# Optimization experiments

Measured on AMD Instinct MI355X. Metric: run time of the kernel, lower is better.

The kernel has to match this reference:

```python
import jax, jax.numpy as jnp
import numpy as np

B, T, D = 64, 512, 512
K_CODES = 256
K_FUTURE = 2


def _gru(x, w_ih, w_hh, b_ih, b_hh):
    # x: [B,T,D]; PyTorch GRU gate order: r, z, n; weights [3D, D]
    xg = jnp.einsum('btd,gd->btg', x, w_ih) + b_ih  # [B,T,3D] precomputed input gates

    def step(h, xg_t):
        hg = h @ w_hh.T + b_hh                      # [B,3D]
        xr, xz, xn = jnp.split(xg_t, 3, axis=-1)
        hr, hz, hn = jnp.split(hg, 3, axis=-1)
        r = jax.nn.sigmoid(xr + hr)
        z = jax.nn.sigmoid(xz + hz)
        n = jnp.tanh(xn + r * hn)
        h_new = (1.0 - z) * n + z * h
        return h_new, h_new

    h0 = jnp.zeros((x.shape[0], w_hh.shape[1]), x.dtype)
    _, hs = jax.lax.scan(step, h0, jnp.swapaxes(xg, 0, 1))
    return jnp.swapaxes(hs, 0, 1)  # [B,T,D]


def setup_inputs() -> dict:
    key = jax.random.key(0)
    ks = jax.random.split(key, 8)
    return {
        'features': jax.random.normal(ks[0], (B, T, D), jnp.float32),
        'codebook': jax.random.uniform(ks[1], (K_CODES, D), jnp.float32, -0.1, 0.1),
        'w_ih': jax.random.normal(ks[2], (3 * D, D), jnp.float32) * 0.02,
        'w_hh': jax.random.normal(ks[3], (3 * D, D), jnp.float32) * 0.02,
        'b_ih': jax.random.normal(ks[4], (3 * D,), jnp.float32) * 0.02,
        'b_hh': jax.random.normal(ks[5], (3 * D,), jnp.float32) * 0.02,
        'proj_w': jax.random.normal(ks[6], (D, D), jnp.float32) * 0.02,
        'proj_b': jax.random.normal(ks[7], (D,), jnp.float32) * 0.02,
    }


def reference(features, codebook, w_ih, w_hh, b_ih, b_hh, proj_w, proj_b):
    b, t, d = features.shape
    # --- quantize: cdist + argmin + gather (squared dists give same argmin) ---
    flat = features.reshape(-1, d)                              # [B*T, D]
    d2 = (jnp.sum(flat * flat, axis=1, keepdims=True)
          - 2.0 * flat @ codebook.T
          + jnp.sum(codebook * codebook, axis=1))               # [B*T, K]
    indices = jnp.argmin(d2, axis=1)                            # [B*T]
    quantized = codebook[indices].reshape(b, t, d)              # gather
    indices = indices.reshape(b, t)

    # --- context prediction loss ---
    hidden = _gru(quantized, w_ih, w_hh, b_ih, b_hh)            # [B,T,D]
    context_proj = hidden @ proj_w.T + proj_b                   # [B,T,D]
    k_max = min(K_FUTURE, t - 1)
    cp_loss = jnp.float32(0.0)
    for k in range(1, k_max + 1):
        cp_loss = cp_loss + jnp.mean((context_proj[:, :-k] - features[:, k:]) ** 2)
    cp_loss = cp_loss / k_max

    # --- VQ loss (stop_gradient mirrors torch .detach()) ---
    commitment_loss = jnp.mean((jax.lax.stop_gradient(features) - quantized) ** 2)
    codebook_loss = jnp.mean((features - jax.lax.stop_gradient(quantized)) ** 2)
    vq_loss = commitment_loss + 0.25 * codebook_loss

    total_loss = cp_loss + vq_loss
    return quantized, indices, total_loss, cp_loss, vq_loss
```

## Files before the change

kernel.cpp:

```cpp
#include <hip/hip_runtime.h>
#include <hip/hip_bf16.h>

#define B_ 64
#define T_ 512
#define D_ 512
#define K_ 256
#define G3 1536

typedef __attribute__((ext_vector_type(8))) short sh8;
typedef __attribute__((ext_vector_type(4))) short sh4;
typedef __attribute__((ext_vector_type(4))) float fx4;
typedef __attribute__((ext_vector_type(4))) int   ix4;

__device__ __forceinline__ short f2bf(float x) {
  __hip_bfloat16 h = __float2bfloat16(x);
  union { __hip_bfloat16 h; short s; } u; u.h = h; return u.s;
}
__device__ __forceinline__ float sigm(float x) { return 1.f / (1.f + __expf(-x)); }
__device__ __forceinline__ float tanh_fast(float x) {
  float e2 = __expf(-2.f * x);
  return (1.f - e2) / (1.f + e2);
}

__global__ void k_cnorm(const float* __restrict__ cb, double* __restrict__ cn) {
  int c = threadIdx.x;
  if (c < K_) {
    double s = 0.0;
    for (int k = 0; k < D_; ++k) { double v = cb[c * D_ + k]; s += v * v; }
    cn[c] = s;
  }
}

__global__ __launch_bounds__(256) void k_cg(const float* __restrict__ cb,
                                            const float* __restrict__ wih,
                                            const float* __restrict__ bih,
                                            const float* __restrict__ bhh,
                                            float* __restrict__ cg) {
  __shared__ float wl[16][512];
  int j0 = blockIdx.x * 16, c0 = blockIdx.y * 64;
  for (int v = threadIdx.x; v < 16 * 128; v += 256) {
    int r = v >> 7, q = v & 127;
    *(fx4*)&wl[r][q * 4] = *(const fx4*)&wih[(j0 + r) * D_ + q * 4];
  }
  __syncthreads();
  for (int p = threadIdx.x; p < 1024; p += 256) {
    int j = p >> 6, c = c0 + (p & 63);
    fx4 a = {0.f, 0.f, 0.f, 0.f};
    const float* cbr = &cb[c * D_];
    for (int q = 0; q < 128; ++q) {
      fx4 w4 = *(fx4*)&wl[j][q * 4];
      fx4 c4 = *(const fx4*)&cbr[q * 4];
      a += w4 * c4;
    }
    int jg = j0 + j;
    float bias = bih[jg] + (jg < 1024 ? bhh[jg] : 0.f);
    cg[c * G3 + jg] = ((a.x + a.y) + (a.z + a.w)) + bias;
  }
}

__global__ void k_cvt(const float* __restrict__ src, __hip_bfloat16* __restrict__ dst, int n4) {
  int i = blockIdx.x * blockDim.x + threadIdx.x;
  if (i < n4) {
    fx4 v = *(const fx4*)&src[i * 4];
    sh4 o; o[0] = f2bf(v.x); o[1] = f2bf(v.y); o[2] = f2bf(v.z); o[3] = f2bf(v.w);
    *(sh4*)&dst[i * 4] = o;
  }
}

__global__ __launch_bounds__(256) void k_quant(const float* __restrict__ feat,
                                               const float* __restrict__ cb,
                                               const double* __restrict__ cn,
                                               int* __restrict__ idxw,
                                               float* __restrict__ outq,
                                               float* __restrict__ outi,
                                               double* __restrict__ lacc) {
  __shared__ float fl[16][516];
  __shared__ double ss1[16][16], ss2[16][16];
  __shared__ int ii1[16][16], ii2[16][16];
  __shared__ int idxl[16];
  __shared__ float rsv[4];
  int row0 = blockIdx.x * 16;
  int tid = threadIdx.x;
  for (int v = tid; v < 16 * 128; v += 256) {
    int r = v >> 7, q = v & 127;
    *(fx4*)&fl[r][q * 4] = *(const fx4*)&feat[(row0 + r) * D_ + q * 4];
  }
  __syncthreads();
  int r = tid & 15, g = tid >> 4;
  fx4 acc[16];
#pragma unroll
  for (int c = 0; c < 16; ++c) acc[c] = (fx4){0.f, 0.f, 0.f, 0.f};
  for (int ch = 0; ch < 8; ++ch) {
    fx4 fc[16];
#pragma unroll
    for (int q = 0; q < 16; ++q) fc[q] = *(fx4*)&fl[r][ch * 64 + q * 4];
#pragma unroll
    for (int c = 0; c < 16; ++c) {
      const float* cbp = &cb[(g * 16 + c) * D_ + ch * 64];
#pragma unroll
      for (int q = 0; q < 16; ++q) {
        fx4 c4 = *(const fx4*)&cbp[q * 4];
        acc[c] += fc[q] * c4;
      }
    }
  }
  double b1 = 1e300, b2 = 1e300; int i1 = 0, i2 = 0;
#pragma unroll
  for (int c = 0; c < 16; ++c) {
    int ci = g * 16 + c;
    double dot = (double)acc[c].x + acc[c].y + acc[c].z + acc[c].w;
    double s = cn[ci] - 2.0 * dot;
    if (s < b1) { b2 = b1; i2 = i1; b1 = s; i1 = ci; }
    else if (s < b2) { b2 = s; i2 = ci; }
  }
  ss1[r][g] = b1; ss2[r][g] = b2; ii1[r][g] = i1; ii2[r][g] = i2;
  __syncthreads();
  if (tid < 16) {
    int rr = tid;
    double c1 = 1e300, c2 = 1e300; int j1 = 0, j2 = 0;
    for (int g2 = 0; g2 < 16; ++g2) {
      double s = ss1[rr][g2]; int ix = ii1[rr][g2];
      if (s < c1 || (s == c1 && ix < j1)) { c2 = c1; j2 = j1; c1 = s; j1 = ix; }
      else if (s < c2 || (s == c2 && ix < j2)) { c2 = s; j2 = ix; }
      s = ss2[rr][g2]; ix = ii2[rr][g2];
      if (s < c1 || (s == c1 && ix < j1)) { c2 = c1; j2 = j1; c1 = s; j1 = ix; }
      else if (s < c2 || (s == c2 && ix < j2)) { c2 = s; j2 = ix; }
    }
    int pick = j1;
    if (c2 - c1 < 1e-4) {
      double d1 = 0.0, d2 = 0.0;
      for (int k = 0; k < D_; ++k) {
        double fv = fl[rr][k];
        d1 += fv * (double)cb[j1 * D_ + k];
        d2 += fv * (double)cb[j2 * D_ + k];
      }
      double e1 = cn[j1] - 2.0 * d1, e2 = cn[j2] - 2.0 * d2;
      if (e2 < e1 || (e2 == e1 && j2 < j1)) pick = j2;
    }
    idxl[rr] = pick;
    idxw[row0 + rr] = pick;
    outi[row0 + rr] = (float)pick;
  }
  __syncthreads();
  float vs = 0.f;
  for (int v = tid; v < 16 * 128; v += 256) {
    int rr = v >> 7, q = v & 127;
    fx4 c4 = *(const fx4*)&cb[idxl[rr] * D_ + q * 4];
    *(fx4*)&outq[(row0 + rr) * D_ + q * 4] = c4;
    fx4 f4 = *(fx4*)&fl[rr][q * 4];
    fx4 d = f4 - c4;
    vs += d.x * d.x + d.y * d.y + d.z * d.z + d.w * d.w;
  }
#pragma unroll
  for (int off = 32; off > 0; off >>= 1) vs += __shfl_down(vs, off);
  if ((tid & 63) == 0) rsv[tid >> 6] = vs;
  __syncthreads();
  if (tid == 0) atomicAdd(&lacc[2], (double)(rsv[0] + rsv[1] + rsv[2] + rsv[3]));
}

__global__ __launch_bounds__(256, 1) void k_gru(const float* __restrict__ whh,
                                                const float* __restrict__ bhh,
                                                const float* __restrict__ cg,
                                                const int* __restrict__ idx,
                                                const __hip_bfloat16* __restrict__ pwb,
                                                const float* __restrict__ pb,
                                                const float* __restrict__ feat,
                                                __hip_bfloat16* __restrict__ hex,
                                                double* __restrict__ lacc,
                                                unsigned int* __restrict__ bar,
                                                unsigned int* __restrict__ coord) {
  int tid = threadIdx.x;
  __shared__ int sh_role, sh_fast;

  if (tid == 0) {
    int xcc = 0;
    asm volatile("s_getreg_b32 %0, hwreg(HW_REG_XCC_ID)" : "=s"(xcc));
    xcc &= 7;
    unsigned slot = __hip_atomic_fetch_add(&coord[xcc], 1u, __ATOMIC_RELAXED,
                                           __HIP_MEMORY_SCOPE_AGENT);
    __hip_atomic_fetch_add(&coord[16], 1u, __ATOMIC_ACQ_REL, __HIP_MEMORY_SCOPE_AGENT);
    while (__hip_atomic_load(&coord[16], __ATOMIC_ACQUIRE, __HIP_MEMORY_SCOPE_AGENT)
           < (unsigned)gridDim.x)
      __builtin_amdgcn_s_sleep(2);
    int role = -1;
    if (slot < 8u) {
      role = xcc * 8 + (int)slot;
    } else {
      for (int x = 0; x < 8 && role < 0; ++x) {
        unsigned cx = __hip_atomic_load(&coord[x], __ATOMIC_RELAXED,
                                        __HIP_MEMORY_SCOPE_AGENT);
        unsigned have = cx < 8u ? cx : 8u;
        if (have < 8u) {
          unsigned s2 = __hip_atomic_fetch_add(&coord[8 + x], 1u, __ATOMIC_RELAXED,
                                               __HIP_MEMORY_SCOPE_AGENT);
          if (s2 < 8u - have) role = x * 8 + (int)(have + s2);
        }
      }
    }
    sh_role = role;
    int fst = 0;
    if (role >= 0) {
      unsigned cgx = __hip_atomic_load(&coord[role >> 3], __ATOMIC_RELAXED,
                                       __HIP_MEMORY_SCOPE_AGENT);
      fst = (cgx >= 8u) ? 1 : 0;
    }
    sh_fast = fst;
    __threadfence();
  }
  __syncthreads();
  const int role = sh_role;
  if (role < 0) return;
  const bool fast = (sh_fast != 0);
  const int g = role >> 3, s = role & 7;

  int w = tid >> 6, lane = tid & 63, l15 = lane & 15, l4 = lane >> 4;

  sh8 A0[16], A1[16], A2[16];
#pragma unroll
  for (int kt = 0; kt < 16; ++kt) {
#pragma unroll
    for (int t3 = 0; t3 < 3; ++t3) {
      int lr = 48 * w + 16 * t3 + l15;
      int gate = lr >> 6, din = lr & 63;
      const float* wr = &whh[(gate * 512 + s * 64 + din) * D_];
      int k0 = kt * 32 + l4 * 8;
      fx4 x = *(const fx4*)&wr[k0];
      fx4 y = *(const fx4*)&wr[k0 + 4];
      sh8 tt;
      tt[0] = f2bf(x.x); tt[1] = f2bf(x.y); tt[2] = f2bf(x.z); tt[3] = f2bf(x.w);
      tt[4] = f2bf(y.x); tt[5] = f2bf(y.y); tt[6] = f2bf(y.z); tt[7] = f2bf(y.w);
      if (t3 == 0) A0[kt] = tt; else if (t3 == 1) A1[kt] = tt; else A2[kt] = tt;
    }
  }
  sh8 P[16];
#pragma unroll
  for (int kt = 0; kt < 16; ++kt)
    P[kt] = *(const sh8*)&pwb[(size_t)(s * 64 + w * 16 + l15) * D_ + kt * 32 + l4 * 8];

  const bool act = (l15 < 8);
  const int bp = l15 & 7;
  const int dgp = s * 64 + w * 16 + l4 * 4;
  fx4 pbv = *(const fx4*)&pb[dgp];

  const int d = tid & 63, b0 = tid >> 6, b1 = b0 + 4;
  const float bn = bhh[1024 + s * 64 + d];

  __shared__ float hg[192][9];
  __shared__ float hl[8][64];
  for (int i = tid; i < 512; i += 256) ((float*)hl)[i] = 0.f;

  unsigned* const barg = &bar[g * 32];
  float s1 = 0.f, s2 = 0.f;

  for (int t = 0; t < T_; ++t) {
    int cur = t & 1, nxt = cur ^ 1;
    int ci0 = idx[(g * 8 + b0) * T_ + t];
    int ci1 = idx[(g * 8 + b1) * T_ + t];
    const float* c0p = &cg[(size_t)ci0 * G3 + s * 64 + d];
    const float* c1p = &cg[(size_t)ci1 * G3 + s * 64 + d];
    float cr0 = c0p[0], cz0 = c0p[512], cn0 = c0p[1024];
    float cr1 = c1p[0], cz1 = c1p[512], cn1 = c1p[1024];

    fx4 a0 = {0, 0, 0, 0}, a1 = {0, 0, 0, 0}, a2 = {0, 0, 0, 0};
    fx4 pacc = {0, 0, 0, 0};
    if (t > 0) {
      const __hip_bfloat16* hb = hex + (size_t)(cur * 8 + g) * 16 * 512;
#pragma unroll
      for (int kt = 0; kt < 16; ++kt) {
        sh8 bfr = *(const sh8*)&hb[l15 * 512 + kt * 32 + l4 * 8];
        a0 = __builtin_amdgcn_mfma_f32_16x16x32_bf16(A0[kt], bfr, a0, 0, 0, 0);
        a1 = __builtin_amdgcn_mfma_f32_16x16x32_bf16(A1[kt], bfr, a1, 0, 0, 0);
        a2 = __builtin_amdgcn_mfma_f32_16x16x32_bf16(A2[kt], bfr, a2, 0, 0, 0);
        pacc = __builtin_amdgcn_mfma_f32_16x16x32_bf16(P[kt], bfr, pacc, 0, 0, 0);
      }
    }
    if (l15 < 8) {
#pragma unroll
      for (int rg = 0; rg < 4; ++rg) {
        hg[48 * w +      l4 * 4 + rg][l15] = a0[rg];
        hg[48 * w + 16 + l4 * 4 + rg][l15] = a1[rg];
        hg[48 * w + 32 + l4 * 4 + rg][l15] = a2[rg];
      }
    }
    __syncthreads();
    {
      float rr = sigm(cr0 + hg[d][b0]);
      float zz = sigm(cz0 + hg[64 + d][b0]);
      float nn = tanh_fast(cn0 + rr * (hg[128 + d][b0] + bn));
      float hv = (1.f - zz) * nn + zz * hl[b0][d];
      hl[b0][d] = hv;
      hex[(size_t)((nxt * 8 + g) * 16 + b0) * 512 + s * 64 + d] = __float2bfloat16(hv);
      rr = sigm(cr1 + hg[d][b1]);
      zz = sigm(cz1 + hg[64 + d][b1]);
      nn = tanh_fast(cn1 + rr * (hg[128 + d][b1] + bn));
      hv = (1.f - zz) * nn + zz * hl[b1][d];
      hl[b1][d] = hv;
      hex[(size_t)((nxt * 8 + g) * 16 + b1) * 512 + s * 64 + d] = __float2bfloat16(hv);
    }
    __syncthreads();
    if (tid == 0) {
      if (!fast) __threadfence();
      __hip_atomic_fetch_add(barg, 1u, __ATOMIC_RELEASE, __HIP_MEMORY_SCOPE_AGENT);
    }
    if (t > 0 && act) {
      fx4 f1 = *(const fx4*)&feat[((size_t)(g * 8 + bp) * T_ + t) * D_ + dgp];
      fx4 v = pacc + pbv;
      fx4 d1 = v - f1;
      s1 += d1.x * d1.x + d1.y * d1.y + d1.z * d1.z + d1.w * d1.w;
      if (t < T_ - 1) {
        fx4 f2 = *(const fx4*)&feat[((size_t)(g * 8 + bp) * T_ + t + 1) * D_ + dgp];
        fx4 d2 = v - f2;
        s2 += d2.x * d2.x + d2.y * d2.y + d2.z * d2.z + d2.w * d2.w;
      }
    }
    if (tid == 0) {
      unsigned tgt = 8u * (unsigned)(t + 1);
      while (__hip_atomic_load(barg, __ATOMIC_ACQUIRE, __HIP_MEMORY_SCOPE_AGENT) < tgt)
        __builtin_amdgcn_s_sleep(1);
      if (!fast) __threadfence();
    }
    __syncthreads();
  }

#pragma unroll
  for (int off = 32; off > 0; off >>= 1) {
    s1 += __shfl_down(s1, off);
    s2 += __shfl_down(s2, off);
  }
  __shared__ float r1[4], r2[4];
  if (lane == 0) { r1[w] = s1; r2[w] = s2; }
  __syncthreads();
  if (tid == 0) {
    atomicAdd(&lacc[0], (double)r1[0] + r1[1] + r1[2] + r1[3]);
    atomicAdd(&lacc[1], (double)r2[0] + r2[1] + r2[2] + r2[3]);
  }
}

__global__ void k_fin(const double* __restrict__ lacc, float* __restrict__ outl) {
  if (threadIdx.x == 0) {
    double cp = 0.5 * (lacc[0] / ((double)B_ * (T_ - 1) * D_) +
                       lacc[1] / ((double)B_ * (T_ - 2) * D_));
    double vq = 1.25 * lacc[2] / ((double)B_ * T_ * D_);
    outl[0] = (float)(cp + vq);
    outl[1] = (float)cp;
    outl[2] = (float)vq;
  }
}

extern "C" void kernel_launch(void* const* d_in, const int* in_sizes, int n_in,
                              void* d_out, int out_size, void* d_ws, size_t ws_size,
                              hipStream_t stream) {
  (void)in_sizes; (void)n_in; (void)out_size; (void)ws_size;
  const float* feat = (const float*)d_in[0];
  const float* cb   = (const float*)d_in[1];
  const float* wih  = (const float*)d_in[2];
  const float* whh  = (const float*)d_in[3];
  const float* bih  = (const float*)d_in[4];
  const float* bhh  = (const float*)d_in[5];
  const float* pw   = (const float*)d_in[6];
  const float* pb   = (const float*)d_in[7];

  float* out  = (float*)d_out;
  float* outq = out;
  float* outi = out + (size_t)B_ * T_ * D_;
  float* outl = outi + B_ * T_;

  char* ws = (char*)d_ws;
  size_t o = 0;
  auto alloc = [&](size_t sz) { void* p = ws + o; o += (sz + 255) & ~(size_t)255; return p; };
  float*          cg    = (float*)alloc(sizeof(float) * K_ * G3);
  double*         cn    = (double*)alloc(sizeof(double) * K_);
  int*            idxw  = (int*)alloc(sizeof(int) * B_ * T_);
  __hip_bfloat16* pwb   = (__hip_bfloat16*)alloc(sizeof(__hip_bfloat16) * D_ * D_);
  double*         lacc  = (double*)alloc(sizeof(double) * 4);
  unsigned*       bar   = (unsigned*)alloc(sizeof(unsigned) * 8 * 32);
  unsigned*       coord = (unsigned*)alloc(sizeof(unsigned) * 32);
  __hip_bfloat16* hex   = (__hip_bfloat16*)alloc(sizeof(__hip_bfloat16) * 2 * 8 * 16 * 512);

  hipMemsetAsync(lacc,  0, sizeof(double) * 4, stream);
  hipMemsetAsync(bar,   0, sizeof(unsigned) * 8 * 32, stream);
  hipMemsetAsync(coord, 0, sizeof(unsigned) * 32, stream);
  hipMemsetAsync(hex,   0, sizeof(__hip_bfloat16) * 2 * 8 * 16 * 512, stream);

  hipLaunchKernelGGL(k_cnorm, dim3(1), dim3(256), 0, stream, cb, cn);
  hipLaunchKernelGGL(k_cg, dim3(96, 4), dim3(256), 0, stream, cb, wih, bih, bhh, cg);
  hipLaunchKernelGGL(k_cvt, dim3(256), dim3(256), 0, stream, pw, pwb, D_ * D_ / 4);
  hipLaunchKernelGGL(k_quant, dim3(2048), dim3(256), 0, stream, feat, cb, cn, idxw, outq, outi, lacc);
  hipLaunchKernelGGL(k_gru, dim3(64), dim3(256), 0, stream, whh, bhh, cg, idxw, pwb, pb, feat, hex, lacc, bar, coord);
  hipLaunchKernelGGL(k_fin, dim3(1), dim3(64), 0, stream, lacc, outl);
}
```

Measured before the change: 3.440 ms.

## Replace per-step group barrier with per-slice flags and rotated K-order consumption

Each of the 8 GRU blocks in a group now publishes its own timestep flag instead of joining a counter barrier. Consumers start the recurrent matmul on their own slice from local shared memory, then poll each peer's flag in rotated order and consume that slice as soon as it is ready. The trailing barrier wait and the extra syncthreads are removed, and feature loads are hoisted ahead of the matmul. This aims to overlap peer latency with MFMA work and shrink the serial sync cost per timestep, at the price of more polling traffic and a subtler memory-ordering protocol. It also relies on the double-buffered hex slots never being overwritten early, since there is no longer a full barrier between steps.

```diff
diff --git a/kernel.cpp b/kernel.cpp
--- a/kernel.cpp
+++ b/kernel.cpp
@@ -167,7 +167,7 @@
                                                 const float* __restrict__ feat,
                                                 __hip_bfloat16* __restrict__ hex,
                                                 double* __restrict__ lacc,
-                                                unsigned int* __restrict__ bar,
+                                                unsigned int* __restrict__ flag,
                                                 unsigned int* __restrict__ coord) {
   int tid = threadIdx.x;
   __shared__ int sh_role, sh_fast;
@@ -215,27 +215,27 @@
 
   int w = tid >> 6, lane = tid & 63, l15 = lane & 15, l4 = lane >> 4;
 
-  sh8 A0[16], A1[16], A2[16];
-#pragma unroll
-  for (int kt = 0; kt < 16; ++kt) {
+  sh8 A0[16], A1[16], A2[16], P[16];
+#pragma unroll
+  for (int p = 0; p < 16; ++p) {
+    int jpos = p >> 1;
+    int j = (s + jpos) & 7;
+    int kt = 2 * j + (p & 1);
+    int k0 = kt * 32 + l4 * 8;
 #pragma unroll
     for (int t3 = 0; t3 < 3; ++t3) {
       int lr = 48 * w + 16 * t3 + l15;
       int gate = lr >> 6, din = lr & 63;
       const float* wr = &whh[(gate * 512 + s * 64 + din) * D_];
-      int k0 = kt * 32 + l4 * 8;
       fx4 x = *(const fx4*)&wr[k0];
       fx4 y = *(const fx4*)&wr[k0 + 4];
       sh8 tt;
       tt[0] = f2bf(x.x); tt[1] = f2bf(x.y); tt[2] = f2bf(x.z); tt[3] = f2bf(x.w);
       tt[4] = f2bf(y.x); tt[5] = f2bf(y.y); tt[6] = f2bf(y.z); tt[7] = f2bf(y.w);
-      if (t3 == 0) A0[kt] = tt; else if (t3 == 1) A1[kt] = tt; else A2[kt] = tt;
-    }
-  }
-  sh8 P[16];
-#pragma unroll
-  for (int kt = 0; kt < 16; ++kt)
-    P[kt] = *(const sh8*)&pwb[(size_t)(s * 64 + w * 16 + l15) * D_ + kt * 32 + l4 * 8];
+      if (t3 == 0) A0[p] = tt; else if (t3 == 1) A1[p] = tt; else A2[p] = tt;
+    }
+    P[p] = *(const sh8*)&pwb[(size_t)(s * 64 + w * 16 + l15) * D_ + k0];
+  }
 
   const bool act = (l15 < 8);
   const int bp = l15 & 7;
@@ -246,10 +246,9 @@
   const float bn = bhh[1024 + s * 64 + d];
 
   __shared__ float hg[192][9];
-  __shared__ float hl[8][64];
-  for (int i = tid; i < 512; i += 256) ((float*)hl)[i] = 0.f;
-
-  unsigned* const barg = &bar[g * 32];
+  __shared__ float hl[8][76];
+  for (int i = tid; i < 8 * 76; i += 256) ((float*)hl)[i] = 0.f;
+
   float s1 = 0.f, s2 = 0.f;
 
   for (int t = 0; t < T_; ++t) {
@@ -260,20 +259,60 @@
     const float* c1p = &cg[(size_t)ci1 * G3 + s * 64 + d];
     float cr0 = c0p[0], cz0 = c0p[512], cn0 = c0p[1024];
     float cr1 = c1p[0], cz1 = c1p[512], cn1 = c1p[1024];
+    fx4 f1 = {0, 0, 0, 0}, f2v = {0, 0, 0, 0};
+    if (t > 0 && act) {
+      f1 = *(const fx4*)&feat[((size_t)(g * 8 + bp) * T_ + t) * D_ + dgp];
+      if (t < T_ - 1)
+        f2v = *(const fx4*)&feat[((size_t)(g * 8 + bp) * T_ + t + 1) * D_ + dgp];
+    }
 
     fx4 a0 = {0, 0, 0, 0}, a1 = {0, 0, 0, 0}, a2 = {0, 0, 0, 0};
     fx4 pacc = {0, 0, 0, 0};
     if (t > 0) {
-      const __hip_bfloat16* hb = hex + (size_t)(cur * 8 + g) * 16 * 512;
-#pragma unroll
-      for (int kt = 0; kt < 16; ++kt) {
-        sh8 bfr = *(const sh8*)&hb[l15 * 512 + kt * 32 + l4 * 8];
-        a0 = __builtin_amdgcn_mfma_f32_16x16x32_bf16(A0[kt], bfr, a0, 0, 0, 0);
-        a1 = __builtin_amdgcn_mfma_f32_16x16x32_bf16(A1[kt], bfr, a1, 0, 0, 0);
-        a2 = __builtin_amdgcn_mfma_f32_16x16x32_bf16(A2[kt], bfr, a2, 0, 0, 0);
-        pacc = __builtin_amdgcn_mfma_f32_16x16x32_bf16(P[kt], bfr, pacc, 0, 0, 0);
-      }
-    }
+      unsigned vch = __hip_atomic_load(&flag[(g * 8 + (lane & 7)) * 32],
+                                       __ATOMIC_ACQUIRE, __HIP_MEMORY_SCOPE_AGENT);
+      unsigned mask = (unsigned)__ballot((int)(vch >= (unsigned)t)) & 0xffu;
+      if (!fast) __threadfence();
+
+#pragma unroll
+      for (int sub = 0; sub < 2; ++sub) {
+        sh8 bfr = {0, 0, 0, 0, 0, 0, 0, 0};
+        if (act) {
+          const float* hp = &hl[bp][sub * 32 + l4 * 8];
+#pragma unroll
+          for (int q = 0; q < 8; ++q) bfr[q] = f2bf(hp[q]);
+        }
+        a0 = __builtin_amdgcn_mfma_f32_16x16x32_bf16(A0[sub], bfr, a0, 0, 0, 0);
+        a1 = __builtin_amdgcn_mfma_f32_16x16x32_bf16(A1[sub], bfr, a1, 0, 0, 0);
+        a2 = __builtin_amdgcn_mfma_f32_16x16x32_bf16(A2[sub], bfr, a2, 0, 0, 0);
+        pacc = __builtin_amdgcn_mfma_f32_16x16x32_bf16(P[sub], bfr, pacc, 0, 0, 0);
+      }
+
+      const __hip_bfloat16* hb = hex + ((size_t)(cur * 8 + g) * 8 + bp) * 512;
+#pragma unroll
+      for (int jj = 1; jj < 8; ++jj) {
+        int j = (s + jj) & 7;
+        if (!((mask >> j) & 1u)) {
+          while (__hip_atomic_load(&flag[(g * 8 + j) * 32], __ATOMIC_ACQUIRE,
+                                   __HIP_MEMORY_SCOPE_AGENT) < (unsigned)t)
+            __builtin_amdgcn_s_sleep(1);
+          if (!fast) __threadfence();
+        }
+        asm volatile("" ::: "memory");
+#pragma unroll
+        for (int sub = 0; sub < 2; ++sub) {
+          int p = 2 * jj + sub;
+          int kt = 2 * j + sub;
+          sh8 bfr = {0, 0, 0, 0, 0, 0, 0, 0};
+          if (act) bfr = *(const sh8*)&hb[kt * 32 + l4 * 8];
+          a0 = __builtin_amdgcn_mfma_f32_16x16x32_bf16(A0[p], bfr, a0, 0, 0, 0);
+          a1 = __builtin_amdgcn_mfma_f32_16x16x32_bf16(A1[p], bfr, a1, 0, 0, 0);
+          a2 = __builtin_amdgcn_mfma_f32_16x16x32_bf16(A2[p], bfr, a2, 0, 0, 0);
+          pacc = __builtin_amdgcn_mfma_f32_16x16x32_bf16(P[p], bfr, pacc, 0, 0, 0);
+        }
+      }
+    }
+
     if (l15 < 8) {
 #pragma unroll
       for (int rg = 0; rg < 4; ++rg) {
@@ -289,37 +328,27 @@
       float nn = tanh_fast(cn0 + rr * (hg[128 + d][b0] + bn));
       float hv = (1.f - zz) * nn + zz * hl[b0][d];
       hl[b0][d] = hv;
-      hex[(size_t)((nxt * 8 + g) * 16 + b0) * 512 + s * 64 + d] = __float2bfloat16(hv);
+      hex[((size_t)(nxt * 8 + g) * 8 + b0) * 512 + s * 64 + d] = __float2bfloat16(hv);
       rr = sigm(cr1 + hg[d][b1]);
       zz = sigm(cz1 + hg[64 + d][b1]);
       nn = tanh_fast(cn1 + rr * (hg[128 + d][b1] + bn));
       hv = (1.f - zz) * nn + zz * hl[b1][d];
       hl[b1][d] = hv;
-      hex[(size_t)((nxt * 8 + g) * 16 + b1) * 512 + s * 64 + d] = __float2bfloat16(hv);
+      hex[((size_t)(nxt * 8 + g) * 8 + b1) * 512 + s * 64 + d] = __float2bfloat16(hv);
     }
     __syncthreads();
-    if (tid == 0) {
-      if (!fast) __threadfence();
-      __hip_atomic_fetch_add(barg, 1u, __ATOMIC_RELEASE, __HIP_MEMORY_SCOPE_AGENT);
-    }
+    if (tid == 0)
+      __hip_atomic_store(&flag[(g * 8 + s) * 32], (unsigned)(t + 1),
+                         __ATOMIC_RELEASE, __HIP_MEMORY_SCOPE_AGENT);
     if (t > 0 && act) {
-      fx4 f1 = *(const fx4*)&feat[((size_t)(g * 8 + bp) * T_ + t) * D_ + dgp];
       fx4 v = pacc + pbv;
       fx4 d1 = v - f1;
       s1 += d1.x * d1.x + d1.y * d1.y + d1.z * d1.z + d1.w * d1.w;
       if (t < T_ - 1) {
-        fx4 f2 = *(const fx4*)&feat[((size_t)(g * 8 + bp) * T_ + t + 1) * D_ + dgp];
-        fx4 d2 = v - f2;
+        fx4 d2 = v - f2v;
         s2 += d2.x * d2.x + d2.y * d2.y + d2.z * d2.z + d2.w * d2.w;
       }
     }
-    if (tid == 0) {
-      unsigned tgt = 8u * (unsigned)(t + 1);
-      while (__hip_atomic_load(barg, __ATOMIC_ACQUIRE, __HIP_MEMORY_SCOPE_AGENT) < tgt)
-        __builtin_amdgcn_s_sleep(1);
-      if (!fast) __threadfence();
-    }
-    __syncthreads();
   }
 
 #pragma unroll
@@ -373,19 +402,18 @@
   int*            idxw  = (int*)alloc(sizeof(int) * B_ * T_);
   __hip_bfloat16* pwb   = (__hip_bfloat16*)alloc(sizeof(__hip_bfloat16) * D_ * D_);
   double*         lacc  = (double*)alloc(sizeof(double) * 4);
-  unsigned*       bar   = (unsigned*)alloc(sizeof(unsigned) * 8 * 32);
+  unsigned*       flag  = (unsigned*)alloc(sizeof(unsigned) * 64 * 32);
   unsigned*       coord = (unsigned*)alloc(sizeof(unsigned) * 32);
-  __hip_bfloat16* hex   = (__hip_bfloat16*)alloc(sizeof(__hip_bfloat16) * 2 * 8 * 16 * 512);
+  __hip_bfloat16* hex   = (__hip_bfloat16*)alloc(sizeof(__hip_bfloat16) * 2 * 8 * 8 * 512);
 
   hipMemsetAsync(lacc,  0, sizeof(double) * 4, stream);
-  hipMemsetAsync(bar,   0, sizeof(unsigned) * 8 * 32, stream);
+  hipMemsetAsync(flag,  0, sizeof(unsigned) * 64 * 32, stream);
   hipMemsetAsync(coord, 0, sizeof(unsigned) * 32, stream);
-  hipMemsetAsync(hex,   0, sizeof(__hip_bfloat16) * 2 * 8 * 16 * 512, stream);
 
   hipLaunchKernelGGL(k_cnorm, dim3(1), dim3(256), 0, stream, cb, cn);
   hipLaunchKernelGGL(k_cg, dim3(96, 4), dim3(256), 0, stream, cb, wih, bih, bhh, cg);
   hipLaunchKernelGGL(k_cvt, dim3(256), dim3(256), 0, stream, pw, pwb, D_ * D_ / 4);
   hipLaunchKernelGGL(k_quant, dim3(2048), dim3(256), 0, stream, feat, cb, cn, idxw, outq, outi, lacc);
-  hipLaunchKernelGGL(k_gru, dim3(64), dim3(256), 0, stream, whh, bhh, cg, idxw, pwb, pb, feat, hex, lacc, bar, coord);
+  hipLaunchKernelGGL(k_gru, dim3(64), dim3(256), 0, stream, whh, bhh, cg, idxw, pwb, pb, feat, hex, lacc, flag, coord);
   hipLaunchKernelGGL(k_fin, dim3(1), dim3(64), 0, stream, lacc, outl);
 }
```

Measured after the change: 5.816 ms. +69.1%, slower.

## Pipeline two batch halves per group with per-slice flags instead of barrier

Applied to the files above, without the earlier changes.

The GRU kernel now uses only 4 XCDs (32 active blocks), with each group handling 16 batch rows split into two interleaved sub-batches of 8. The per-step group barrier is replaced by per-slice release flags that consumers poll with a wave-wide vote, so one sub-batch's recurrence can proceed while the other's exchange is still settling. The hidden-state exchange buffer gains a 4-deep ring to avoid overwrite hazards, and wave priority is raised. This is meant to hide cross-block synchronisation latency, at the cost of halving the active CUs and doubling the serial phases per block.

```diff
diff --git a/kernel.cpp b/kernel.cpp
--- a/kernel.cpp
+++ b/kernel.cpp
@@ -167,7 +167,7 @@
                                                 const float* __restrict__ feat,
                                                 __hip_bfloat16* __restrict__ hex,
                                                 double* __restrict__ lacc,
-                                                unsigned int* __restrict__ bar,
+                                                unsigned int* __restrict__ flag,
                                                 unsigned int* __restrict__ coord) {
   int tid = threadIdx.x;
   __shared__ int sh_role, sh_fast;
@@ -182,11 +182,12 @@
     while (__hip_atomic_load(&coord[16], __ATOMIC_ACQUIRE, __HIP_MEMORY_SCOPE_AGENT)
            < (unsigned)gridDim.x)
       __builtin_amdgcn_s_sleep(2);
-    int role = -1;
-    if (slot < 8u) {
+    int role = -1, fst = 0;
+    if (xcc < 4 && slot < 8u) {
       role = xcc * 8 + (int)slot;
+      fst = 1;
     } else {
-      for (int x = 0; x < 8 && role < 0; ++x) {
+      for (int x = 0; x < 4 && role < 0; ++x) {
         unsigned cx = __hip_atomic_load(&coord[x], __ATOMIC_RELAXED,
                                         __HIP_MEMORY_SCOPE_AGENT);
         unsigned have = cx < 8u ? cx : 8u;
@@ -198,12 +199,6 @@
       }
     }
     sh_role = role;
-    int fst = 0;
-    if (role >= 0) {
-      unsigned cgx = __hip_atomic_load(&coord[role >> 3], __ATOMIC_RELAXED,
-                                       __HIP_MEMORY_SCOPE_AGENT);
-      fst = (cgx >= 8u) ? 1 : 0;
-    }
     sh_fast = fst;
     __threadfence();
   }
@@ -213,6 +208,7 @@
   const bool fast = (sh_fast != 0);
   const int g = role >> 3, s = role & 7;
 
+  __builtin_amdgcn_s_setprio(1);
   int w = tid >> 6, lane = tid & 63, l15 = lane & 15, l4 = lane >> 4;
 
   sh8 A0[16], A1[16], A2[16];
@@ -246,16 +242,16 @@
   const float bn = bhh[1024 + s * 64 + d];
 
   __shared__ float hg[192][9];
-  __shared__ float hl[8][64];
-  for (int i = tid; i < 512; i += 256) ((float*)hl)[i] = 0.f;
-
-  unsigned* const barg = &bar[g * 32];
+  __shared__ float hl[16][64];
+  for (int i = tid; i < 16 * 64; i += 256) ((float*)hl)[i] = 0.f;
+
   float s1 = 0.f, s2 = 0.f;
 
-  for (int t = 0; t < T_; ++t) {
-    int cur = t & 1, nxt = cur ^ 1;
-    int ci0 = idx[(g * 8 + b0) * T_ + t];
-    int ci1 = idx[(g * 8 + b1) * T_ + t];
+  for (int ph = 0; ph < 2 * T_; ++ph) {
+    int sub = ph & 1, t = ph >> 1;
+    int bb = g * 16 + sub * 8;
+    int ci0 = idx[(bb + b0) * T_ + t];
+    int ci1 = idx[(bb + b1) * T_ + t];
     const float* c0p = &cg[(size_t)ci0 * G3 + s * 64 + d];
     const float* c1p = &cg[(size_t)ci1 * G3 + s * 64 + d];
     float cr0 = c0p[0], cz0 = c0p[512], cn0 = c0p[1024];
@@ -264,10 +260,21 @@
     fx4 a0 = {0, 0, 0, 0}, a1 = {0, 0, 0, 0}, a2 = {0, 0, 0, 0};
     fx4 pacc = {0, 0, 0, 0};
     if (t > 0) {
-      const __hip_bfloat16* hb = hex + (size_t)(cur * 8 + g) * 16 * 512;
+      const unsigned* fp = &flag[(g * 2 + sub) * 32 + (lane & 7)];
+      for (;;) {
+        unsigned v = __hip_atomic_load(fp, __ATOMIC_RELAXED, __HIP_MEMORY_SCOPE_AGENT);
+        if (__all((int)(v >= (unsigned)t))) break;
+        __builtin_amdgcn_s_sleep(1);
+      }
+      asm volatile("" ::: "memory");
+      if (!fast) __threadfence();
+
+      const __hip_bfloat16* hb =
+          hex + ((((size_t)((t - 1) & 3) * 4 + g) * 2 + sub) * 8 + bp) * 512;
 #pragma unroll
       for (int kt = 0; kt < 16; ++kt) {
-        sh8 bfr = *(const sh8*)&hb[l15 * 512 + kt * 32 + l4 * 8];
+        sh8 bfr = {0, 0, 0, 0, 0, 0, 0, 0};
+        if (act) bfr = *(const sh8*)&hb[kt * 32 + l4 * 8];
         a0 = __builtin_amdgcn_mfma_f32_16x16x32_bf16(A0[kt], bfr, a0, 0, 0, 0);
         a1 = __builtin_amdgcn_mfma_f32_16x16x32_bf16(A1[kt], bfr, a1, 0, 0, 0);
         a2 = __builtin_amdgcn_mfma_f32_16x16x32_bf16(A2[kt], bfr, a2, 0, 0, 0);
@@ -284,42 +291,38 @@
     }
     __syncthreads();
     {
+      __hip_bfloat16* hw =
+          hex + (((size_t)(t & 3) * 4 + g) * 2 + sub) * 8 * 512 + s * 64 + d;
       float rr = sigm(cr0 + hg[d][b0]);
       float zz = sigm(cz0 + hg[64 + d][b0]);
       float nn = tanh_fast(cn0 + rr * (hg[128 + d][b0] + bn));
-      float hv = (1.f - zz) * nn + zz * hl[b0][d];
-      hl[b0][d] = hv;
-      hex[(size_t)((nxt * 8 + g) * 16 + b0) * 512 + s * 64 + d] = __float2bfloat16(hv);
+      float hv = (1.f - zz) * nn + zz * hl[sub * 8 + b0][d];
+      hl[sub * 8 + b0][d] = hv;
+      hw[(size_t)b0 * 512] = __float2bfloat16(hv);
       rr = sigm(cr1 + hg[d][b1]);
       zz = sigm(cz1 + hg[64 + d][b1]);
       nn = tanh_fast(cn1 + rr * (hg[128 + d][b1] + bn));
-      hv = (1.f - zz) * nn + zz * hl[b1][d];
-      hl[b1][d] = hv;
-      hex[(size_t)((nxt * 8 + g) * 16 + b1) * 512 + s * 64 + d] = __float2bfloat16(hv);
+      hv = (1.f - zz) * nn + zz * hl[sub * 8 + b1][d];
+      hl[sub * 8 + b1][d] = hv;
+      hw[(size_t)b1 * 512] = __float2bfloat16(hv);
     }
     __syncthreads();
     if (tid == 0) {
       if (!fast) __threadfence();
-      __hip_atomic_fetch_add(barg, 1u, __ATOMIC_RELEASE, __HIP_MEMORY_SCOPE_AGENT);
+      __hip_atomic_store(&flag[(g * 2 + sub) * 32 + s], (unsigned)(t + 1),
+                         __ATOMIC_RELEASE, __HIP_MEMORY_SCOPE_AGENT);
     }
     if (t > 0 && act) {
-      fx4 f1 = *(const fx4*)&feat[((size_t)(g * 8 + bp) * T_ + t) * D_ + dgp];
       fx4 v = pacc + pbv;
+      fx4 f1 = *(const fx4*)&feat[((size_t)(bb + bp) * T_ + t) * D_ + dgp];
       fx4 d1 = v - f1;
       s1 += d1.x * d1.x + d1.y * d1.y + d1.z * d1.z + d1.w * d1.w;
       if (t < T_ - 1) {
-        fx4 f2 = *(const fx4*)&feat[((size_t)(g * 8 + bp) * T_ + t + 1) * D_ + dgp];
+        fx4 f2 = *(const fx4*)&feat[((size_t)(bb + bp) * T_ + t + 1) * D_ + dgp];
         fx4 d2 = v - f2;
         s2 += d2.x * d2.x + d2.y * d2.y + d2.z * d2.z + d2.w * d2.w;
       }
     }
-    if (tid == 0) {
-      unsigned tgt = 8u * (unsigned)(t + 1);
-      while (__hip_atomic_load(barg, __ATOMIC_ACQUIRE, __HIP_MEMORY_SCOPE_AGENT) < tgt)
-        __builtin_amdgcn_s_sleep(1);
-      if (!fast) __threadfence();
-    }
-    __syncthreads();
   }
 
 #pragma unroll
@@ -373,19 +376,18 @@
   int*            idxw  = (int*)alloc(sizeof(int) * B_ * T_);
   __hip_bfloat16* pwb   = (__hip_bfloat16*)alloc(sizeof(__hip_bfloat16) * D_ * D_);
   double*         lacc  = (double*)alloc(sizeof(double) * 4);
-  unsigned*       bar   = (unsigned*)alloc(sizeof(unsigned) * 8 * 32);
+  unsigned*       flag  = (unsigned*)alloc(sizeof(unsigned) * 8 * 32);
   unsigned*       coord = (unsigned*)alloc(sizeof(unsigned) * 32);
-  __hip_bfloat16* hex   = (__hip_bfloat16*)alloc(sizeof(__hip_bfloat16) * 2 * 8 * 16 * 512);
+  __hip_bfloat16* hex   = (__hip_bfloat16*)alloc(sizeof(__hip_bfloat16) * 4 * 4 * 2 * 8 * 512);
 
   hipMemsetAsync(lacc,  0, sizeof(double) * 4, stream);
-  hipMemsetAsync(bar,   0, sizeof(unsigned) * 8 * 32, stream);
+  hipMemsetAsync(flag,  0, sizeof(unsigned) * 8 * 32, stream);
   hipMemsetAsync(coord, 0, sizeof(unsigned) * 32, stream);
-  hipMemsetAsync(hex,   0, sizeof(__hip_bfloat16) * 2 * 8 * 16 * 512, stream);
 
   hipLaunchKernelGGL(k_cnorm, dim3(1), dim3(256), 0, stream, cb, cn);
   hipLaunchKernelGGL(k_cg, dim3(96, 4), dim3(256), 0, stream, cb, wih, bih, bhh, cg);
   hipLaunchKernelGGL(k_cvt, dim3(256), dim3(256), 0, stream, pw, pwb, D_ * D_ / 4);
   hipLaunchKernelGGL(k_quant, dim3(2048), dim3(256), 0, stream, feat, cb, cn, idxw, outq, outi, lacc);
-  hipLaunchKernelGGL(k_gru, dim3(64), dim3(256), 0, stream, whh, bhh, cg, idxw, pwb, pb, feat, hex, lacc, bar, coord);
+  hipLaunchKernelGGL(k_gru, dim3(64), dim3(256), 0, stream, whh, bhh, cg, idxw, pwb, pb, feat, hex, lacc, flag, coord);
   hipLaunchKernelGGL(k_fin, dim3(1), dim3(64), 0, stream, lacc, outl);
 }
```

New measurement: 5.081 ms. +47.7%, slower.
